# Optimization experiments

Hardware: AMD Instinct MI355X
Metric: run time of the kernel (lower is better)

Reference implementation:

```python
import jax, jax.numpy as jnp
import numpy as np

N, DIM, QK, HEADS, NWIN, TOPK = 1, 128, 128, 8, 8, 4
D = H = W = 32


def setup_inputs() -> dict:
    key = jax.random.key(0)
    ks = jax.random.split(key, 3)
    s = lambda fan: 1.0 / np.sqrt(fan)
    return {
        "x": jax.random.normal(ks[0], (N, D, H, W, DIM), jnp.float32),
        "w_qkv": jax.random.normal(ks[1], (DIM, 2 * QK + DIM), jnp.float32) * s(DIM),
        "b_qkv": jnp.zeros((2 * QK + DIM,), jnp.float32),
        "w_o": jax.random.normal(ks[2], (DIM, DIM), jnp.float32) * s(DIM),
        "b_o": jnp.zeros((DIM,), jnp.float32),
    }


def _forward(x, w_qkv, b_qkv, w_o, b_o):
    n, Dd, Hh, Ww, C = x.shape
    d, h, w = Dd // NWIN, Hh // NWIN, Ww // NWIN
    p3, w3 = NWIN ** 3, d * h * w
    cq, cv = QK // HEADS, DIM // HEADS
    scale = QK ** -0.5
    # window partition: n (q d)(j h)(i w) c -> n (q j i) d h w c
    xw = x.reshape(n, NWIN, d, NWIN, h, NWIN, w, C)
    xw = xw.transpose(0, 1, 3, 5, 2, 4, 6, 7).reshape(n, p3, d, h, w, C)
    # fused qkv projection
    qkv = xw @ w_qkv + b_qkv
    q, k, v = qkv[..., :QK], qkv[..., QK:2 * QK], qkv[..., 2 * QK:]
    q_pix = q.reshape(n, p3, w3, QK)
    kv_pix = jnp.concatenate([k, v], axis=-1).reshape(n, p3, w3, QK + DIM)
    # region-level routing (non-differentiable: detached in original)
    q_win = jax.lax.stop_gradient(q.mean((2, 3, 4)))  # (n, p3, QK)
    k_win = jax.lax.stop_gradient(k.mean((2, 3, 4)))
    logits = jnp.einsum('npc,nqc->npq', q_win * scale, k_win)  # (n, p3, p3)
    _, r_idx = jax.lax.top_k(logits, TOPK)  # (n, p3, topk)
    # gather top-k regions' KV per query window: (n, p3, topk, w3, QK+DIM)
    kv_sel = jax.vmap(lambda kvp, idx: kvp[idx])(kv_pix, r_idx)
    k_sel = kv_sel[..., :QK].reshape(n * p3, TOPK * w3, HEADS, cq).transpose(0, 2, 3, 1)  # (np3, m, cq, k*w3)
    v_sel = kv_sel[..., QK:].reshape(n * p3, TOPK * w3, HEADS, cv).transpose(0, 2, 1, 3)  # (np3, m, k*w3, cv)
    qh = q_pix.reshape(n * p3, w3, HEADS, cq).transpose(0, 2, 1, 3)  # (np3, m, w3, cq)
    attn = jax.nn.softmax((qh * scale) @ k_sel, axis=-1)  # (np3, m, w3, k*w3)
    out = attn @ v_sel  # (np3, m, w3, cv)
    # (n q j i) m (d h w) c -> n (q d)(j h)(i w)(m c)
    out = out.reshape(n, NWIN, NWIN, NWIN, HEADS, d, h, w, cv)
    out = out.transpose(0, 1, 5, 2, 6, 3, 7, 4, 8).reshape(n, Dd, Hh, Ww, DIM)
    out = out @ w_o + b_o
    return out, q, k, v


def reference(x, w_qkv, b_qkv, w_o, b_o):
    return _forward(x, w_qkv, b_qkv, w_o, b_o)
```

## Files before the change

### kernel.cpp

```cpp
#include <hip/hip_runtime.h>
#include <cmath>

namespace {

typedef __attribute__((ext_vector_type(8))) short short8;
typedef __attribute__((ext_vector_type(4))) float f32x4;
typedef __attribute__((ext_vector_type(4))) unsigned u32x4;

constexpr float kScale = 0.08838834764831845f;

__device__ __forceinline__ int voxel_row(int p, int pix) {
  int pd = p >> 6, ph = (p >> 3) & 7, pw = p & 7;
  int iz = pix >> 4, iy = (pix >> 2) & 3, ix = pix & 3;
  return (((pd * 4 + iz) * 32 + (ph * 4 + iy)) * 32 + (pw * 4 + ix));
}

__device__ __forceinline__ float dot4(float4 a, float4 b) {
  return a.x * b.x + a.y * b.y + a.z * b.z + a.w * b.w;
}

__device__ __forceinline__ short bf16c(float f) {
  unsigned u = __builtin_bit_cast(unsigned, f);
  u += 0x7fffu + ((u >> 16) & 1u);
  return (short)(u >> 16);
}

__device__ __forceinline__ unsigned bfpack(float lo, float hi) {
  return (unsigned)(unsigned short)bf16c(lo) |
         ((unsigned)(unsigned short)bf16c(hi) << 16);
}

__device__ __forceinline__ short8 cvt8(const float* src) {
  float4 a = *(const float4*)src, b = *(const float4*)(src + 4);
  short8 o;
  o[0] = bf16c(a.x); o[1] = bf16c(a.y); o[2] = bf16c(a.z); o[3] = bf16c(a.w);
  o[4] = bf16c(b.x); o[5] = bf16c(b.y); o[6] = bf16c(b.z); o[7] = bf16c(b.w);
  return o;
}

__device__ __forceinline__ short8 cvt8s(const float* src, float sc) {
  float4 a = *(const float4*)src, b = *(const float4*)(src + 4);
  short8 o;
  o[0] = bf16c(a.x * sc); o[1] = bf16c(a.y * sc);
  o[2] = bf16c(a.z * sc); o[3] = bf16c(a.w * sc);
  o[4] = bf16c(b.x * sc); o[5] = bf16c(b.y * sc);
  o[6] = bf16c(b.z * sc); o[7] = bf16c(b.w * sc);
  return o;
}

__global__ __launch_bounds__(64) void k_pack(
    const float* __restrict__ w, short* __restrict__ dst, int N) {
  const int lane = threadIdx.x;
  const int ntile = blockIdx.x >> 2, ks = blockIdx.x & 3;
  const int k0 = ks * 32 + (lane >> 4) * 8, col = ntile * 16 + (lane & 15);
  short8 o;
#pragma unroll
  for (int i = 0; i < 8; ++i) o[i] = bf16c(w[(size_t)(k0 + i) * N + col]);
  *(short8*)(dst + ((size_t)blockIdx.x * 64 + lane) * 8) = o;
}

__global__ __launch_bounds__(256) void k_qkv(
    const float* __restrict__ x, const short* __restrict__ wpk,
    const float* __restrict__ bias, const float* __restrict__ wfull,
    float* __restrict__ q, float* __restrict__ k, float* __restrict__ v,
    short* __restrict__ vt, short* __restrict__ kbh,
    float* __restrict__ qwin, float* __restrict__ kwin) {
  __shared__ short sX[64][136];
  __shared__ float xpart[16][16][8];
  __shared__ float xm[128];
  const int p = blockIdx.x, t = threadIdx.x;
  const int wave = t >> 6, lane = t & 63, l15 = lane & 15, lg = lane >> 4;

  float ps[8] = {0.f, 0.f, 0.f, 0.f, 0.f, 0.f, 0.f, 0.f};
#pragma unroll
  for (int r = 0; r < 4; ++r) {
    int unit = t + r * 256;
    int row = unit >> 4, u = unit & 15;
    const float* src = x + (size_t)voxel_row(p, row) * 128 + u * 8;
    float4 a = *(const float4*)src, b = *(const float4*)(src + 4);
    ps[0] += a.x; ps[1] += a.y; ps[2] += a.z; ps[3] += a.w;
    ps[4] += b.x; ps[5] += b.y; ps[6] += b.z; ps[7] += b.w;
    short8 o;
    o[0] = bf16c(a.x); o[1] = bf16c(a.y); o[2] = bf16c(a.z); o[3] = bf16c(a.w);
    o[4] = bf16c(b.x); o[5] = bf16c(b.y); o[6] = bf16c(b.z); o[7] = bf16c(b.w);
    *(short8*)(&sX[row][u * 8]) = o;
  }
#pragma unroll
  for (int i = 0; i < 8; ++i) xpart[t >> 4][t & 15][i] = ps[i];
  __syncthreads();
  if (t < 128) {
    float s = 0.f;
#pragma unroll
    for (int g = 0; g < 16; ++g) s += xpart[g][t >> 3][t & 7];
    xm[t] = s * (1.f / 64.f);
  }
  __syncthreads();

  f32x4 acc[4][6];
#pragma unroll
  for (int mt = 0; mt < 4; ++mt)
#pragma unroll
    for (int nt = 0; nt < 6; ++nt) acc[mt][nt] = f32x4{0.f, 0.f, 0.f, 0.f};
#pragma unroll
  for (int ks = 0; ks < 4; ++ks) {
    short8 a[4];
#pragma unroll
    for (int mt = 0; mt < 4; ++mt)
      a[mt] = *(const short8*)(&sX[mt * 16 + l15][ks * 32 + lg * 8]);
#pragma unroll
    for (int nt = 0; nt < 6; ++nt) {
      int ntg = wave * 6 + nt;
      short8 b = *(const short8*)(wpk + ((size_t)(ntg * 4 + ks) * 64 + lane) * 8);
#pragma unroll
      for (int mt = 0; mt < 4; ++mt)
        acc[mt][nt] = __builtin_amdgcn_mfma_f32_16x16x32_bf16(a[mt], b, acc[mt][nt], 0, 0, 0);
    }
  }
#pragma unroll
  for (int nt = 0; nt < 6; ++nt) {
    int n = (wave * 6 + nt) * 16 + l15;
    float bv = bias[n];
    float* dst = n < 128 ? q : (n < 256 ? k : v);
    int col = n & 127;
#pragma unroll
    for (int mt = 0; mt < 4; ++mt) {
      float o0 = acc[mt][nt][0] + bv, o1 = acc[mt][nt][1] + bv;
      float o2 = acc[mt][nt][2] + bv, o3 = acc[mt][nt][3] + bv;
      int row0 = mt * 16 + lg * 4;
      dst[(size_t)(p * 64 + row0 + 0) * 128 + col] = o0;
      dst[(size_t)(p * 64 + row0 + 1) * 128 + col] = o1;
      dst[(size_t)(p * 64 + row0 + 2) * 128 + col] = o2;
      dst[(size_t)(p * 64 + row0 + 3) * 128 + col] = o3;
      if (n >= 256) {
        uint2 pk;
        pk.x = bfpack(o0, o1);
        pk.y = bfpack(o2, o3);
        *(uint2*)(vt + (size_t)p * 8192 + (size_t)(n - 256) * 64 + row0) = pk;
      } else if (n >= 128) {
        int hh = (n - 128) >> 4, d = (n - 128) & 15;
        short* kd = kbh + (((size_t)(p * 8 + hh)) * 64 + row0) * 16 + d;
        kd[0] = bf16c(o0);
        kd[16] = bf16c(o1);
        kd[32] = bf16c(o2);
        kd[48] = bf16c(o3);
      }
    }
  }

  {
    float acc2 = bias[t];
    for (int kk = 0; kk < 128; ++kk)
      acc2 = fmaf(xm[kk], wfull[(size_t)kk * 384 + t], acc2);
    if (t < 128) qwin[p * 128 + t] = acc2;
    else kwin[p * 128 + (t - 128)] = acc2;
  }
}

__global__ __launch_bounds__(256) void k_route(
    const float* __restrict__ qwin, const float* __restrict__ kwin,
    int* __restrict__ ridx) {
  __shared__ float qs[128];
  __shared__ float lg[512];
  __shared__ float rv[256];
  __shared__ int ri[256];
  const int p = blockIdx.x, t = threadIdx.x;
  if (t < 32) *(float4*)(&qs[t * 4]) = *(const float4*)(qwin + p * 128 + t * 4);
  __syncthreads();
  for (int jj = t; jj < 512; jj += 256) {
    const float* kr = kwin + (size_t)jj * 128;
    float s = 0.f;
    for (int c = 0; c < 128; c += 4) {
      float4 k4 = *(const float4*)(kr + c);
      float4 q4 = *(const float4*)(qs + c);
      s += dot4(q4, k4);
    }
    lg[jj] = s;
  }
  __syncthreads();
  for (int sel = 0; sel < 4; ++sel) {
    float bv = lg[t];
    int bi = t;
    float v2 = lg[t + 256];
    if (v2 > bv) { bv = v2; bi = t + 256; }
    rv[t] = bv; ri[t] = bi;
    __syncthreads();
    for (int off = 128; off > 0; off >>= 1) {
      if (t < off && rv[t + off] > rv[t]) { rv[t] = rv[t + off]; ri[t] = ri[t + off]; }
      __syncthreads();
    }
    if (t == 0) { ridx[p * 4 + sel] = ri[0]; lg[ri[0]] = -INFINITY; }
    __syncthreads();
  }
}

__global__ __launch_bounds__(256, 4) void k_attn(
    const float* __restrict__ q, const short* __restrict__ kbh,
    const short* __restrict__ vt, const int* __restrict__ ridx,
    float* __restrict__ ao) {
  const int bid = blockIdx.x, t = threadIdx.x;
  const int p = bid >> 1, half = bid & 1;
  const int wave = t >> 6, lane = t & 63;
  const int l15 = lane & 15, lg = lane >> 4;
  const int h = half * 4 + wave;

  const int4 ws4 = *(const int4*)(ridx + p * 4);
  const int wsa[4] = {ws4.x, ws4.y, ws4.z, ws4.w};

  const int src0 = ((lg & 1) << 5) | l15;
  const int src1 = src0 + 16;

  short8 qf[4];
#pragma unroll
  for (int nt = 0; nt < 4; ++nt) {
    if (lg < 2)
      qf[nt] = cvt8s(q + ((size_t)(p * 64 + nt * 16 + l15)) * 128 + h * 16 + lg * 8, kScale);
    else
      qf[nt] = short8{0, 0, 0, 0, 0, 0, 0, 0};
  }

  float m_r[4] = {-1e30f, -1e30f, -1e30f, -1e30f};
  float l_r[4] = {0.f, 0.f, 0.f, 0.f};
  f32x4 oacc[4];
#pragma unroll
  for (int i = 0; i < 4; ++i) oacc[i] = f32x4{0.f, 0.f, 0.f, 0.f};

#pragma unroll
  for (int c = 0; c < 4; ++c) {
    const int wsel = wsa[c];
    const short* kw = kbh + ((size_t)(wsel * 8 + h)) * 1024;
    short8 af[4];
#pragma unroll
    for (int mt = 0; mt < 4; ++mt) {
      if (lg < 2)
        af[mt] = *(const short8*)(kw + (mt * 16 + l15) * 16 + lg * 8);
      else
        af[mt] = short8{0, 0, 0, 0, 0, 0, 0, 0};
    }
    const short* vw = vt + (size_t)wsel * 8192 + (size_t)(h * 16 + l15) * 64 + lg * 8;
    short8 av0 = *(const short8*)(vw);
    short8 av1 = *(const short8*)(vw + 32);

#pragma unroll
    for (int nt = 0; nt < 4; ++nt) {
      f32x4 s[4];
#pragma unroll
      for (int mt = 0; mt < 4; ++mt)
        s[mt] = __builtin_amdgcn_mfma_f32_16x16x32_bf16(
            af[mt], qf[nt], f32x4{0.f, 0.f, 0.f, 0.f}, 0, 0, 0);
      float mx = -1e30f;
#pragma unroll
      for (int mt = 0; mt < 4; ++mt)
#pragma unroll
        for (int j = 0; j < 4; ++j) mx = fmaxf(mx, s[mt][j]);
      mx = fmaxf(mx, __shfl_xor(mx, 16));
      mx = fmaxf(mx, __shfl_xor(mx, 32));
      float mnew = fmaxf(m_r[nt], mx);
      float sc = __expf(m_r[nt] - mnew);
      m_r[nt] = mnew;
      float ls = 0.f;
#pragma unroll
      for (int mt = 0; mt < 4; ++mt)
#pragma unroll
        for (int j = 0; j < 4; ++j) {
          float e = __expf(s[mt][j] - mnew);
          s[mt][j] = e;
          ls += e;
        }
      ls += __shfl_xor(ls, 16);
      ls += __shfl_xor(ls, 32);
      l_r[nt] = l_r[nt] * sc + ls;
      oacc[nt][0] *= sc; oacc[nt][1] *= sc;
      oacc[nt][2] *= sc; oacc[nt][3] *= sc;
      unsigned P2[4][2];
#pragma unroll
      for (int mt = 0; mt < 4; ++mt) {
        P2[mt][0] = bfpack(s[mt][0], s[mt][1]);
        P2[mt][1] = bfpack(s[mt][2], s[mt][3]);
      }
#pragma unroll
      for (int kt = 0; kt < 2; ++kt) {
        unsigned lo0 = (unsigned)__shfl((int)P2[2 * kt + 0][0], src0);
        unsigned hi0 = (unsigned)__shfl((int)P2[2 * kt + 1][0], src0);
        unsigned lo1 = (unsigned)__shfl((int)P2[2 * kt + 0][1], src0);
        unsigned hi1 = (unsigned)__shfl((int)P2[2 * kt + 1][1], src0);
        unsigned lo2 = (unsigned)__shfl((int)P2[2 * kt + 0][0], src1);
        unsigned hi2 = (unsigned)__shfl((int)P2[2 * kt + 1][0], src1);
        unsigned lo3 = (unsigned)__shfl((int)P2[2 * kt + 0][1], src1);
        unsigned hi3 = (unsigned)__shfl((int)P2[2 * kt + 1][1], src1);
        u32x4 bw;
        bw[0] = (lg < 2) ? lo0 : hi0;
        bw[1] = (lg < 2) ? lo1 : hi1;
        bw[2] = (lg < 2) ? lo2 : hi2;
        bw[3] = (lg < 2) ? lo3 : hi3;
        short8 bfr = __builtin_bit_cast(short8, bw);
        oacc[nt] = __builtin_amdgcn_mfma_f32_16x16x32_bf16(
            kt == 0 ? av0 : av1, bfr, oacc[nt], 0, 0, 0);
      }
    }
  }

#pragma unroll
  for (int nt = 0; nt < 4; ++nt) {
    float inv = 1.f / l_r[nt];
    float4 st;
    st.x = oacc[nt][0] * inv; st.y = oacc[nt][1] * inv;
    st.z = oacc[nt][2] * inv; st.w = oacc[nt][3] * inv;
    int qpix = nt * 16 + l15;
    *(float4*)(ao + (size_t)voxel_row(p, qpix) * 128 + h * 16 + lg * 4) = st;
  }
}

__global__ __launch_bounds__(256) void k_proj(
    float* io, const short* __restrict__ wpk, const float* __restrict__ bias) {
  __shared__ short sX[64][136];
  const int p = blockIdx.x, t = threadIdx.x;
  const int wave = t >> 6, lane = t & 63, l15 = lane & 15, lg = lane >> 4;
#pragma unroll
  for (int r = 0; r < 4; ++r) {
    int unit = t + r * 256;
    int row = unit >> 4, u = unit & 15;
    *(short8*)(&sX[row][u * 8]) =
        cvt8(io + (size_t)voxel_row(p, row) * 128 + u * 8);
  }
  __syncthreads();
  f32x4 acc[4][2];
#pragma unroll
  for (int mt = 0; mt < 4; ++mt) {
    acc[mt][0] = f32x4{0.f, 0.f, 0.f, 0.f};
    acc[mt][1] = f32x4{0.f, 0.f, 0.f, 0.f};
  }
#pragma unroll
  for (int ks = 0; ks < 4; ++ks) {
    short8 a[4];
#pragma unroll
    for (int mt = 0; mt < 4; ++mt)
      a[mt] = *(const short8*)(&sX[mt * 16 + l15][ks * 32 + lg * 8]);
#pragma unroll
    for (int nt = 0; nt < 2; ++nt) {
      int ntg = wave * 2 + nt;
      short8 b = *(const short8*)(wpk + ((size_t)(ntg * 4 + ks) * 64 + lane) * 8);
#pragma unroll
      for (int mt = 0; mt < 4; ++mt)
        acc[mt][nt] = __builtin_amdgcn_mfma_f32_16x16x32_bf16(a[mt], b, acc[mt][nt], 0, 0, 0);
    }
  }
#pragma unroll
  for (int nt = 0; nt < 2; ++nt) {
    int n = (wave * 2 + nt) * 16 + l15;
    float bv = bias[n];
#pragma unroll
    for (int mt = 0; mt < 4; ++mt)
#pragma unroll
      for (int j = 0; j < 4; ++j)
        io[(size_t)voxel_row(p, mt * 16 + lg * 4 + j) * 128 + n] = acc[mt][nt][j] + bv;
  }
}

}

extern "C" void kernel_launch(void* const* d_in, const int* in_sizes, int n_in,
                              void* d_out, int out_size, void* d_ws, size_t ws_size,
                              hipStream_t stream) {
  (void)in_sizes; (void)n_in; (void)out_size; (void)ws_size;
  const float* x = (const float*)d_in[0];
  const float* w_qkv = (const float*)d_in[1];
  const float* b_qkv = (const float*)d_in[2];
  const float* w_o = (const float*)d_in[3];
  const float* b_o = (const float*)d_in[4];

  float* out = (float*)d_out;
  float* q = out + 4194304;
  float* k = q + 4194304;
  float* v = k + 4194304;

  float* qwin = (float*)d_ws;
  float* kwin = qwin + 65536;
  int* ridx = (int*)(kwin + 65536);
  short* wpk_qkv = (short*)(ridx + 2048);
  short* wpk_o = wpk_qkv + 49152;
  short* vt = wpk_o + 16384;
  short* kbh = vt + 4194304;

  k_pack<<<96, 64, 0, stream>>>(w_qkv, wpk_qkv, 384);
  k_pack<<<32, 64, 0, stream>>>(w_o, wpk_o, 128);
  k_qkv<<<512, 256, 0, stream>>>(x, wpk_qkv, b_qkv, w_qkv, q, k, v, vt, kbh, qwin, kwin);
  k_route<<<512, 256, 0, stream>>>(qwin, kwin, ridx);
  k_attn<<<1024, 256, 0, stream>>>(q, kbh, vt, ridx, out);
  k_proj<<<512, 256, 0, stream>>>(out, wpk_o, b_o);
}
```

Measured before the change: 88.22 us.

## Stage bf16 Q and attention output in window-major layouts, merge pack kernels

The QKV kernel now also writes a pre-scaled bf16 Q in per-window, per-head layout, so attention loads short8 Q fragments directly instead of reading fp32 Q and converting it. Attention writes its output as bf16 in window-major order to a scratch buffer. The projection kernel reads its MFMA A operands straight from that buffer, dropping the LDS staging and the fp32 round trip through the output tensor. Attention also switches to one 512-thread block per window, and the two weight-pack launches become one. This costs extra writes in the QKV kernel plus more workspace, and rounds the attention output to bf16 before projection.

Measured after the change: 87.63 us. No clear change (-0.7%).

```diff
diff --git a/kernel.cpp b/kernel.cpp
--- a/kernel.cpp
+++ b/kernel.cpp
@@ -38,32 +38,31 @@
   return o;
 }
 
-__device__ __forceinline__ short8 cvt8s(const float* src, float sc) {
-  float4 a = *(const float4*)src, b = *(const float4*)(src + 4);
-  short8 o;
-  o[0] = bf16c(a.x * sc); o[1] = bf16c(a.y * sc);
-  o[2] = bf16c(a.z * sc); o[3] = bf16c(a.w * sc);
-  o[4] = bf16c(b.x * sc); o[5] = bf16c(b.y * sc);
-  o[6] = bf16c(b.z * sc); o[7] = bf16c(b.w * sc);
-  return o;
-}
-
-__global__ __launch_bounds__(64) void k_pack(
-    const float* __restrict__ w, short* __restrict__ dst, int N) {
+__global__ __launch_bounds__(64) void k_pack2(
+    const float* __restrict__ wqkv, const float* __restrict__ wo,
+    short* __restrict__ dstq, short* __restrict__ dsto) {
   const int lane = threadIdx.x;
-  const int ntile = blockIdx.x >> 2, ks = blockIdx.x & 3;
+  const float* w;
+  short* dst;
+  int fid, N;
+  if (blockIdx.x < 96) {
+    w = wqkv; dst = dstq; fid = blockIdx.x; N = 384;
+  } else {
+    w = wo; dst = dsto; fid = blockIdx.x - 96; N = 128;
+  }
+  const int ntile = fid >> 2, ks = fid & 3;
   const int k0 = ks * 32 + (lane >> 4) * 8, col = ntile * 16 + (lane & 15);
   short8 o;
 #pragma unroll
   for (int i = 0; i < 8; ++i) o[i] = bf16c(w[(size_t)(k0 + i) * N + col]);
-  *(short8*)(dst + ((size_t)blockIdx.x * 64 + lane) * 8) = o;
+  *(short8*)(dst + ((size_t)fid * 64 + lane) * 8) = o;
 }
 
 __global__ __launch_bounds__(256) void k_qkv(
     const float* __restrict__ x, const short* __restrict__ wpk,
     const float* __restrict__ bias, const float* __restrict__ wfull,
     float* __restrict__ q, float* __restrict__ k, float* __restrict__ v,
-    short* __restrict__ vt, short* __restrict__ kbh,
+    short* __restrict__ vt, short* __restrict__ kbh, short* __restrict__ qbh,
     float* __restrict__ qwin, float* __restrict__ kwin) {
   __shared__ short sX[64][136];
   __shared__ float xpart[16][16][8];
@@ -143,6 +142,13 @@
         kd[16] = bf16c(o1);
         kd[32] = bf16c(o2);
         kd[48] = bf16c(o3);
+      } else {
+        int hh = n >> 4, d = n & 15;
+        short* qd = qbh + (((size_t)(p * 8 + hh)) * 64 + row0) * 16 + d;
+        qd[0] = bf16c(o0 * kScale);
+        qd[16] = bf16c(o1 * kScale);
+        qd[32] = bf16c(o2 * kScale);
+        qd[48] = bf16c(o3 * kScale);
       }
     }
   }
@@ -193,15 +199,13 @@
   }
 }
 
-__global__ __launch_bounds__(256, 4) void k_attn(
-    const float* __restrict__ q, const short* __restrict__ kbh,
+__global__ __launch_bounds__(512, 4) void k_attn(
+    const short* __restrict__ qbh, const short* __restrict__ kbh,
     const short* __restrict__ vt, const int* __restrict__ ridx,
-    float* __restrict__ ao) {
-  const int bid = blockIdx.x, t = threadIdx.x;
-  const int p = bid >> 1, half = bid & 1;
-  const int wave = t >> 6, lane = t & 63;
+    short* __restrict__ aob) {
+  const int p = blockIdx.x, t = threadIdx.x;
+  const int h = t >> 6, lane = t & 63;
   const int l15 = lane & 15, lg = lane >> 4;
-  const int h = half * 4 + wave;
 
   const int4 ws4 = *(const int4*)(ridx + p * 4);
   const int wsa[4] = {ws4.x, ws4.y, ws4.z, ws4.w};
@@ -209,11 +213,12 @@
   const int src0 = ((lg & 1) << 5) | l15;
   const int src1 = src0 + 16;
 
+  const short* qw = qbh + ((size_t)(p * 8 + h)) * 1024;
   short8 qf[4];
 #pragma unroll
   for (int nt = 0; nt < 4; ++nt) {
     if (lg < 2)
-      qf[nt] = cvt8s(q + ((size_t)(p * 64 + nt * 16 + l15)) * 128 + h * 16 + lg * 8, kScale);
+      qf[nt] = *(const short8*)(qw + (nt * 16 + l15) * 16 + lg * 8);
     else
       qf[nt] = short8{0, 0, 0, 0, 0, 0, 0, 0};
   }
@@ -302,27 +307,19 @@
 #pragma unroll
   for (int nt = 0; nt < 4; ++nt) {
     float inv = 1.f / l_r[nt];
-    float4 st;
-    st.x = oacc[nt][0] * inv; st.y = oacc[nt][1] * inv;
-    st.z = oacc[nt][2] * inv; st.w = oacc[nt][3] * inv;
+    uint2 pk;
+    pk.x = bfpack(oacc[nt][0] * inv, oacc[nt][1] * inv);
+    pk.y = bfpack(oacc[nt][2] * inv, oacc[nt][3] * inv);
     int qpix = nt * 16 + l15;
-    *(float4*)(ao + (size_t)voxel_row(p, qpix) * 128 + h * 16 + lg * 4) = st;
+    *(uint2*)(aob + ((size_t)(p * 64 + qpix)) * 128 + h * 16 + lg * 4) = pk;
   }
 }
 
 __global__ __launch_bounds__(256) void k_proj(
-    float* io, const short* __restrict__ wpk, const float* __restrict__ bias) {
-  __shared__ short sX[64][136];
+    const short* __restrict__ aob, const short* __restrict__ wpk,
+    const float* __restrict__ bias, float* __restrict__ out) {
   const int p = blockIdx.x, t = threadIdx.x;
   const int wave = t >> 6, lane = t & 63, l15 = lane & 15, lg = lane >> 4;
-#pragma unroll
-  for (int r = 0; r < 4; ++r) {
-    int unit = t + r * 256;
-    int row = unit >> 4, u = unit & 15;
-    *(short8*)(&sX[row][u * 8]) =
-        cvt8(io + (size_t)voxel_row(p, row) * 128 + u * 8);
-  }
-  __syncthreads();
   f32x4 acc[4][2];
 #pragma unroll
   for (int mt = 0; mt < 4; ++mt) {
@@ -334,7 +331,7 @@
     short8 a[4];
 #pragma unroll
     for (int mt = 0; mt < 4; ++mt)
-      a[mt] = *(const short8*)(&sX[mt * 16 + l15][ks * 32 + lg * 8]);
+      a[mt] = *(const short8*)(aob + ((size_t)(p * 64 + mt * 16 + l15)) * 128 + ks * 32 + lg * 8);
 #pragma unroll
     for (int nt = 0; nt < 2; ++nt) {
       int ntg = wave * 2 + nt;
@@ -352,7 +349,7 @@
     for (int mt = 0; mt < 4; ++mt)
 #pragma unroll
       for (int j = 0; j < 4; ++j)
-        io[(size_t)voxel_row(p, mt * 16 + lg * 4 + j) * 128 + n] = acc[mt][nt][j] + bv;
+        out[(size_t)voxel_row(p, mt * 16 + lg * 4 + j) * 128 + n] = acc[mt][nt][j] + bv;
   }
 }
 
@@ -380,11 +377,12 @@
   short* wpk_o = wpk_qkv + 49152;
   short* vt = wpk_o + 16384;
   short* kbh = vt + 4194304;
-
-  k_pack<<<96, 64, 0, stream>>>(w_qkv, wpk_qkv, 384);
-  k_pack<<<32, 64, 0, stream>>>(w_o, wpk_o, 128);
-  k_qkv<<<512, 256, 0, stream>>>(x, wpk_qkv, b_qkv, w_qkv, q, k, v, vt, kbh, qwin, kwin);
+  short* qbh = kbh + 4194304;
+  short* aob = qbh + 4194304;
+
+  k_pack2<<<128, 64, 0, stream>>>(w_qkv, w_o, wpk_qkv, wpk_o);
+  k_qkv<<<512, 256, 0, stream>>>(x, wpk_qkv, b_qkv, w_qkv, q, k, v, vt, kbh, qbh, qwin, kwin);
   k_route<<<512, 256, 0, stream>>>(qwin, kwin, ridx);
-  k_attn<<<1024, 256, 0, stream>>>(q, kbh, vt, ridx, out);
-  k_proj<<<512, 256, 0, stream>>>(out, wpk_o, b_o);
-}
+  k_attn<<<512, 512, 0, stream>>>(qbh, kbh, vt, ridx, aob);
+  k_proj<<<512, 256, 0, stream>>>(aob, wpk_o, b_o, out);
+}
```
